# Kernel tuning notes

Hardware: AMD Instinct MI355X
Metric: run time of the kernel (lower is better)

The kernel has to match this reference:

```python
import jax, jax.numpy as jnp
import numpy as np

MULTI_N_NUM = 2  # hardcoded in FCR.__init__
EPS = 1e-07


def setup_inputs() -> dict:
    key = jax.random.key(0)
    ka, kp, kn, ki = jax.random.split(key, 4)
    B, C, H, W = 32, 3, 256, 256
    a = jax.random.normal(ka, (B, C, H, W), dtype=jnp.float32)
    p = jax.random.normal(kp, (B, C, H, W), dtype=jnp.float32)
    n = jax.random.normal(kn, (B, C, H, W), dtype=jnp.float32)
    # sample_with_j(B, 2, i) -> [i, random j != i]; deterministic materialization
    offs = jax.random.randint(ki, (B, MULTI_N_NUM - 1), 1, B)  # in [1, B-1]
    base = jnp.arange(B, dtype=jnp.int64)
    other = (base[:, None] + offs.astype(jnp.int64)) % B
    neg_idx = jnp.concatenate([base[:, None], other], axis=1)  # [B, 2]
    return {"a": a, "p": p, "n": n, "neg_idx": neg_idx}


def reference(a, p, n, neg_idx):
    # FFT2 over the last two dims -> complex64
    a_fft = jnp.fft.fft2(a)
    p_fft = jnp.fft.fft2(p)
    n_fft = jnp.fft.fft2(n)
    # d_ap[i] = mean |a_fft[i] - p_fft[i]| over (C, H, W)
    d_ap = jnp.mean(jnp.abs(a_fft - p_fft), axis=(1, 2, 3))  # [B]
    # d_an[i, k] = mean |a_fft[i] - n_fft[neg_idx[i, k]]|
    n_gather = n_fft[neg_idx]                                  # [B, K, C, H, W]
    d_an = jnp.mean(jnp.abs(a_fft[:, None] - n_gather), axis=(2, 3, 4))  # [B, K]
    contrastive = jnp.sum(d_ap[:, None] / (d_an + EPS))
    return contrastive / (MULTI_N_NUM * a.shape[0])
```

## Files before the change

### kernel.cpp

```cpp
#include <hip/hip_runtime.h>
#include <hip/hip_fp16.h>
#include <math.h>

#define PIDX(e) ((e) + ((e) >> 4))

#define WAVE_SYNC()                          \
    do {                                     \
        __builtin_amdgcn_wave_barrier();     \
        asm volatile("" ::: "memory");       \
    } while (0)

__device__ __forceinline__ float2 cadd(float2 a, float2 b) { return {a.x + b.x, a.y + b.y}; }
__device__ __forceinline__ float2 csub(float2 a, float2 b) { return {a.x - b.x, a.y - b.y}; }
__device__ __forceinline__ float2 cmul(float2 a, float2 b) {
    return {a.x * b.x - a.y * b.y, a.x * b.y + a.y * b.x};
}
__device__ __forceinline__ float2 shfl64(float2 v, int src) {
    return {__shfl(v.x, src), __shfl(v.y, src)};
}

#define BFLY4(c0, c1, c2, c3, d0, d1, d2, d3)            \
    {                                                    \
        float2 sa = cadd(c0, c2);                        \
        float2 sb = csub(c0, c2);                        \
        float2 sc = cadd(c1, c3);                        \
        float2 sd = {(c1).y - (c3).y, (c3).x - (c1).x}; \
        d0 = cadd(sa, sc);                               \
        d1 = cadd(sb, sd);                               \
        d2 = csub(sa, sc);                               \
        d3 = csub(sb, sd);                               \
    }

struct Tw {
    float2 w1, w2, w3;
};
__device__ __forceinline__ Tw make_tw(int idx) {
    const float ang = -0.024543692606170259f * (float)idx;
    float sy, cx;
    __sincosf(ang, &sy, &cx);
    Tw tw;
    tw.w1 = {cx, sy};
    tw.w2 = cmul(tw.w1, tw.w1);
    tw.w3 = cmul(tw.w2, tw.w1);
    return tw;
}

__device__ __forceinline__ void fft_stage0(float2 z0, float2 z1, float2 z2, float2 z3, float2* X,
                                           int t, const Tw& tw) {
    float2 d0, d1, d2, d3;
    BFLY4(z0, z1, z2, z3, d0, d1, d2, d3);
    const int ob = t << 2;
    X[PIDX(ob)] = d0;
    X[PIDX(ob + 1)] = cmul(tw.w1, d1);
    X[PIDX(ob + 2)] = cmul(tw.w2, d2);
    X[PIDX(ob + 3)] = cmul(tw.w3, d3);
    WAVE_SYNC();
}

template <int SH>
__device__ __forceinline__ void fft_stage_mid(float2* X, int t, const Tw& tw) {
    float2 c0 = X[PIDX(t)];
    float2 c1 = X[PIDX(t + 64)];
    float2 c2 = X[PIDX(t + 128)];
    float2 c3 = X[PIDX(t + 192)];
    WAVE_SYNC();
    float2 d0, d1, d2, d3;
    BFLY4(c0, c1, c2, c3, d0, d1, d2, d3);
    const int mm = 1 << SH;
    const int jj = t >> SH;
    const int kk = t & (mm - 1);
    const int ob = kk + 4 * mm * jj;
    X[PIDX(ob)] = d0;
    X[PIDX(ob + mm)] = cmul(tw.w1, d1);
    X[PIDX(ob + 2 * mm)] = cmul(tw.w2, d2);
    X[PIDX(ob + 3 * mm)] = cmul(tw.w3, d3);
    WAVE_SYNC();
}

__device__ __forceinline__ void fft_stage3_reg(float2* X, int t, float2& d0, float2& d1,
                                               float2& d2, float2& d3) {
    float2 c0 = X[PIDX(t)];
    float2 c1 = X[PIDX(t + 64)];
    float2 c2 = X[PIDX(t + 128)];
    float2 c3 = X[PIDX(t + 192)];
    WAVE_SYNC();
    BFLY4(c0, c1, c2, c3, d0, d1, d2, d3);
}

__device__ __forceinline__ void load16(const float* __restrict__ abase,
                                       const float* __restrict__ sbase, int r, int t, float* a0,
                                       float* a1, float* s0, float* s1) {
#pragma unroll
    for (int q = 0; q < 4; ++q) {
        a0[q] = abase[(r << 8) + t + (q << 6)];
        a1[q] = abase[((r + 1) << 8) + t + (q << 6)];
        s0[q] = sbase[(r << 8) + t + (q << 6)];
        s1[q] = sbase[((r + 1) << 8) + t + (q << 6)];
    }
}

__global__ __launch_bounds__(256) void k_rowfft(const float* __restrict__ A,
                                                const float* __restrict__ P,
                                                const float* __restrict__ N,
                                                const int* __restrict__ negIdx,
                                                __half2* __restrict__ ws, int img0) {
    __shared__ float2 Xb[4][272];
    __shared__ __half2 outT[128 * 33];

    const int img = img0 + blockIdx.y;
    const int pair = img / 3;
    const int ch = img - pair * 3;
    int i, jn;
    const float* S;
    if (pair < 32) {
        i = pair;
        jn = pair;
        S = P;
    } else {
        const int t2 = pair - 32;
        i = t2 >> 1;
        jn = negIdx[(i << 1) + (t2 & 1)];
        S = N;
    }
    const float* abase = A + ((size_t)(i * 3 + ch) << 16);
    const float* sbase = S + ((size_t)(jn * 3 + ch) << 16);

    const int tid = threadIdx.x;
    const int w = tid >> 6;
    const int t = tid & 63;
    const int r0 = blockIdx.x * 32;

    const Tw tw0 = make_tw(t);
    const Tw tw1 = make_tw(t & ~3);
    const Tw tw2 = make_tw(t & ~15);
    const int ridx = (64 - t) & 63;

    float pa0[4], pa1[4], ps0[4], ps1[4];
    load16(abase, sbase, r0 + 2 * w, t, pa0, pa1, ps0, ps1);

    for (int it = 0; it < 4; ++it) {
        const int slot = 2 * (it * 4 + w);
        float2 z[4];
#pragma unroll
        for (int q = 0; q < 4; ++q) z[q] = {pa0[q] - ps0[q], pa1[q] - ps1[q]};
        if (it < 3) load16(abase, sbase, r0 + 2 * ((it + 1) * 4 + w), t, pa0, pa1, ps0, ps1);
        fft_stage0(z[0], z[1], z[2], z[3], Xb[w], t, tw0);
        fft_stage_mid<2>(Xb[w], t, tw1);
        fft_stage_mid<4>(Xb[w], t, tw2);
        float2 d0, d1, d2, d3;
        fft_stage3_reg(Xb[w], t, d0, d1, d2, d3);
        const float2 m3 = shfl64(d3, ridx);
        const float2 m2 = shfl64(d2, ridx);
        if (t == 0) {
            outT[slot] = __floats2half2_rn(d0.x, d2.x);
            outT[slot + 1] = __floats2half2_rn(d0.y, d2.y);
        } else {
            outT[t * 33 + slot] = __floats2half2_rn(0.5f * (d0.x + m3.x), 0.5f * (d0.y - m3.y));
            outT[t * 33 + slot + 1] =
                __floats2half2_rn(0.5f * (d0.y + m3.y), -0.5f * (d0.x - m3.x));
        }
        {
            const int v = t + 64;
            const float2 mm2 = (t == 0) ? d3 : m2;
            outT[v * 33 + slot] = __floats2half2_rn(0.5f * (d1.x + mm2.x), 0.5f * (d1.y - mm2.y));
            outT[v * 33 + slot + 1] =
                __floats2half2_rn(0.5f * (d1.y + mm2.y), -0.5f * (d1.x - mm2.x));
        }
        WAVE_SYNC();
    }

    __syncthreads();

    __half2* g = ws + (size_t)blockIdx.y * (128 * 256);
    for (int e = tid; e < 128 * 8; e += 256) {
        const int v = e >> 3, rl4 = (e & 7) << 2;
        float4 val;
        __half2* vp = (__half2*)&val;
#pragma unroll
        for (int k = 0; k < 4; ++k) vp[k] = outT[v * 33 + rl4 + k];
        *(float4*)(g + v * 256 + r0 + rl4) = val;
    }
}

__global__ __launch_bounds__(256) void k_colfft(const __half2* __restrict__ ws,
                                                float* __restrict__ partial, int img0) {
    __shared__ float2 Xb[4][272];
    __shared__ float wsum[4];
    const int tid = threadIdx.x;
    const int w = tid >> 6, t = tid & 63;
    const int vbase = blockIdx.x * 16 + w * 4;
    const __half2* gimg = ws + (size_t)blockIdx.y * (128 * 256);

    const Tw tw0 = make_tw(t);
    const Tw tw1 = make_tw(t & ~3);
    const Tw tw2 = make_tw(t & ~15);

    float acc = 0.f;
    __half2 cur[4], nxt[4];
#pragma unroll
    for (int q = 0; q < 4; ++q) cur[q] = gimg[(size_t)vbase * 256 + t + (q << 6)];
    for (int j = 0; j < 4; ++j) {
        const int v = vbase + j;
        if (j < 3) {
#pragma unroll
            for (int q = 0; q < 4; ++q) nxt[q] = gimg[(size_t)(v + 1) * 256 + t + (q << 6)];
        }
        float2 z[4];
#pragma unroll
        for (int q = 0; q < 4; ++q) z[q] = __half22float2(cur[q]);
        fft_stage0(z[0], z[1], z[2], z[3], Xb[w], t, tw0);
        fft_stage_mid<2>(Xb[w], t, tw1);
        fft_stage_mid<4>(Xb[w], t, tw2);
        float2 d0, d1, d2, d3;
        fft_stage3_reg(Xb[w], t, d0, d1, d2, d3);
        float ssum = 0.f;
        if (v == 0) {
            Xb[w][PIDX(t)] = d0;
            Xb[w][PIDX(t + 64)] = d1;
            Xb[w][PIDX(t + 128)] = d2;
            Xb[w][PIDX(t + 192)] = d3;
            WAVE_SYNC();
#pragma unroll
            for (int q = 0; q < 4; ++q) {
                const int u = t + 64 * q;
                const float2 zu = Xb[w][PIDX(u)];
                const float2 zm = Xb[w][PIDX((256 - u) & 255)];
                const float ax = 0.5f * (zu.x + zm.x), ay = 0.5f * (zu.y - zm.y);
                const float bx = 0.5f * (zu.y + zm.y), by = -0.5f * (zu.x - zm.x);
                ssum += sqrtf(ax * ax + ay * ay) + sqrtf(bx * bx + by * by);
            }
        } else {
            ssum = 2.f * (sqrtf(d0.x * d0.x + d0.y * d0.y) + sqrtf(d1.x * d1.x + d1.y * d1.y) +
                          sqrtf(d2.x * d2.x + d2.y * d2.y) + sqrtf(d3.x * d3.x + d3.y * d3.y));
        }
        acc += ssum;
#pragma unroll
        for (int q = 0; q < 4; ++q) cur[q] = nxt[q];
        WAVE_SYNC();
    }
#pragma unroll
    for (int off = 32; off; off >>= 1) acc += __shfl_down(acc, off);
    if (t == 0) wsum[w] = acc;
    __syncthreads();
    if (tid == 0) {
        const int img = img0 + blockIdx.y;
        partial[img * 8 + blockIdx.x] = wsum[0] + wsum[1] + wsum[2] + wsum[3];
    }
}

__global__ void k_final(const float* __restrict__ partial, float* __restrict__ out) {
    __shared__ float ps[96];
    const int t = threadIdx.x;
    if (t < 96) {
        float s = 0.f;
        const float* p = partial + t * 24;
        for (int e = 0; e < 24; ++e) s += p[e];
        ps[t] = s;
    }
    __syncthreads();
    if (t < 64) {
        const float inv = 1.f / 196608.f;
        const float dap = ps[t >> 1] * inv;
        const float dan = ps[32 + t] * inv + 1e-7f;
        float val = dap / dan;
#pragma unroll
        for (int off = 32; off; off >>= 1) val += __shfl_down(val, off);
        if (t == 0) out[0] = val * (1.f / 64.f);
    }
}

extern "C" void kernel_launch(void* const* d_in, const int* in_sizes, int n_in,
                              void* d_out, int out_size, void* d_ws, size_t ws_size,
                              hipStream_t stream) {
    const float* A = (const float*)d_in[0];
    const float* P = (const float*)d_in[1];
    const float* N = (const float*)d_in[2];
    const int* negIdx = (const int*)d_in[3];

    float* partial = (float*)d_ws;
    __half2* inter = (__half2*)((char*)d_ws + 40960);
    const size_t perImg = (size_t)128 * 256 * sizeof(__half2);
    size_t avail = ws_size > 40960 ? ws_size - 40960 : 0;
    int cap = (int)(avail / perImg);
    if (cap > 288) cap = 288;
    if (cap < 1) cap = 1;

    for (int img0 = 0; img0 < 288; img0 += cap) {
        const int nimg = (288 - img0 < cap) ? (288 - img0) : cap;
        dim3 g1(8, nimg);
        k_rowfft<<<g1, dim3(256), 0, stream>>>(A, P, N, negIdx, inter, img0);
        dim3 g2(8, nimg);
        k_colfft<<<g2, dim3(256), 0, stream>>>(inter, partial, img0);
    }
    k_final<<<1, 128, 0, stream>>>(partial, (float*)d_out);
}
```

Baseline: 45.72 us.

## Fuse row and column FFT into one per-image kernel using LDS spectrum

Merges the row-FFT and column-FFT kernels into one kernel where each 512-thread block handles a whole image. The half-precision intermediate spectrum is kept in shared memory (about 131 KB) rather than written to and re-read from global workspace, and the partial sums shrink to one per image. This removes the global round trip and a kernel launch, but only 288 blocks run with very large LDS use, so occupancy is at most one block per CU and the column loads no longer prefetch ahead.

```diff
diff --git a/kernel.cpp b/kernel.cpp
--- a/kernel.cpp
+++ b/kernel.cpp
@@ -99,15 +99,16 @@
     }
 }
 
-__global__ __launch_bounds__(256) void k_rowfft(const float* __restrict__ A,
-                                                const float* __restrict__ P,
-                                                const float* __restrict__ N,
-                                                const int* __restrict__ negIdx,
-                                                __half2* __restrict__ ws, int img0) {
-    __shared__ float2 Xb[4][272];
-    __shared__ __half2 outT[128 * 33];
-
-    const int img = img0 + blockIdx.y;
+__global__ __launch_bounds__(512) void k_fused(const float* __restrict__ A,
+                                               const float* __restrict__ P,
+                                               const float* __restrict__ N,
+                                               const int* __restrict__ negIdx,
+                                               float* __restrict__ partial) {
+    __shared__ __half2 spec[128 * 257];
+    __shared__ float2 Xb[8][272];
+    __shared__ float wsum[8];
+
+    const int img = blockIdx.x;
     const int pair = img / 3;
     const int ch = img - pair * 3;
     int i, jn;
@@ -128,7 +129,6 @@
     const int tid = threadIdx.x;
     const int w = tid >> 6;
     const int t = tid & 63;
-    const int r0 = blockIdx.x * 32;
 
     const Tw tw0 = make_tw(t);
     const Tw tw1 = make_tw(t & ~3);
@@ -136,14 +136,14 @@
     const int ridx = (64 - t) & 63;
 
     float pa0[4], pa1[4], ps0[4], ps1[4];
-    load16(abase, sbase, r0 + 2 * w, t, pa0, pa1, ps0, ps1);
-
-    for (int it = 0; it < 4; ++it) {
-        const int slot = 2 * (it * 4 + w);
+    load16(abase, sbase, 2 * w, t, pa0, pa1, ps0, ps1);
+
+    for (int it = 0; it < 16; ++it) {
+        const int p = it * 8 + w;
         float2 z[4];
 #pragma unroll
         for (int q = 0; q < 4; ++q) z[q] = {pa0[q] - ps0[q], pa1[q] - ps1[q]};
-        if (it < 3) load16(abase, sbase, r0 + 2 * ((it + 1) * 4 + w), t, pa0, pa1, ps0, ps1);
+        if (it < 15) load16(abase, sbase, 2 * ((it + 1) * 8 + w), t, pa0, pa1, ps0, ps1);
         fft_stage0(z[0], z[1], z[2], z[3], Xb[w], t, tw0);
         fft_stage_mid<2>(Xb[w], t, tw1);
         fft_stage_mid<4>(Xb[w], t, tw2);
@@ -151,19 +151,20 @@
         fft_stage3_reg(Xb[w], t, d0, d1, d2, d3);
         const float2 m3 = shfl64(d3, ridx);
         const float2 m2 = shfl64(d2, ridx);
+        const int r = 2 * p;
         if (t == 0) {
-            outT[slot] = __floats2half2_rn(d0.x, d2.x);
-            outT[slot + 1] = __floats2half2_rn(d0.y, d2.y);
+            spec[r] = __floats2half2_rn(d0.x, d2.x);
+            spec[r + 1] = __floats2half2_rn(d0.y, d2.y);
         } else {
-            outT[t * 33 + slot] = __floats2half2_rn(0.5f * (d0.x + m3.x), 0.5f * (d0.y - m3.y));
-            outT[t * 33 + slot + 1] =
+            spec[t * 257 + r] = __floats2half2_rn(0.5f * (d0.x + m3.x), 0.5f * (d0.y - m3.y));
+            spec[t * 257 + r + 1] =
                 __floats2half2_rn(0.5f * (d0.y + m3.y), -0.5f * (d0.x - m3.x));
         }
         {
             const int v = t + 64;
             const float2 mm2 = (t == 0) ? d3 : m2;
-            outT[v * 33 + slot] = __floats2half2_rn(0.5f * (d1.x + mm2.x), 0.5f * (d1.y - mm2.y));
-            outT[v * 33 + slot + 1] =
+            spec[v * 257 + r] = __floats2half2_rn(0.5f * (d1.x + mm2.x), 0.5f * (d1.y - mm2.y));
+            spec[v * 257 + r + 1] =
                 __floats2half2_rn(0.5f * (d1.y + mm2.y), -0.5f * (d1.x - mm2.x));
         }
         WAVE_SYNC();
@@ -171,43 +172,12 @@
 
     __syncthreads();
 
-    __half2* g = ws + (size_t)blockIdx.y * (128 * 256);
-    for (int e = tid; e < 128 * 8; e += 256) {
-        const int v = e >> 3, rl4 = (e & 7) << 2;
-        float4 val;
-        __half2* vp = (__half2*)&val;
-#pragma unroll
-        for (int k = 0; k < 4; ++k) vp[k] = outT[v * 33 + rl4 + k];
-        *(float4*)(g + v * 256 + r0 + rl4) = val;
-    }
-}
-
-__global__ __launch_bounds__(256) void k_colfft(const __half2* __restrict__ ws,
-                                                float* __restrict__ partial, int img0) {
-    __shared__ float2 Xb[4][272];
-    __shared__ float wsum[4];
-    const int tid = threadIdx.x;
-    const int w = tid >> 6, t = tid & 63;
-    const int vbase = blockIdx.x * 16 + w * 4;
-    const __half2* gimg = ws + (size_t)blockIdx.y * (128 * 256);
-
-    const Tw tw0 = make_tw(t);
-    const Tw tw1 = make_tw(t & ~3);
-    const Tw tw2 = make_tw(t & ~15);
-
     float acc = 0.f;
-    __half2 cur[4], nxt[4];
-#pragma unroll
-    for (int q = 0; q < 4; ++q) cur[q] = gimg[(size_t)vbase * 256 + t + (q << 6)];
-    for (int j = 0; j < 4; ++j) {
-        const int v = vbase + j;
-        if (j < 3) {
-#pragma unroll
-            for (int q = 0; q < 4; ++q) nxt[q] = gimg[(size_t)(v + 1) * 256 + t + (q << 6)];
-        }
+    for (int it = 0; it < 16; ++it) {
+        const int v = it * 8 + w;
         float2 z[4];
 #pragma unroll
-        for (int q = 0; q < 4; ++q) z[q] = __half22float2(cur[q]);
+        for (int q = 0; q < 4; ++q) z[q] = __half22float2(spec[v * 257 + t + (q << 6)]);
         fft_stage0(z[0], z[1], z[2], z[3], Xb[w], t, tw0);
         fft_stage_mid<2>(Xb[w], t, tw1);
         fft_stage_mid<4>(Xb[w], t, tw2);
@@ -234,8 +204,6 @@
                           sqrtf(d2.x * d2.x + d2.y * d2.y) + sqrtf(d3.x * d3.x + d3.y * d3.y));
         }
         acc += ssum;
-#pragma unroll
-        for (int q = 0; q < 4; ++q) cur[q] = nxt[q];
         WAVE_SYNC();
     }
 #pragma unroll
@@ -243,20 +211,17 @@
     if (t == 0) wsum[w] = acc;
     __syncthreads();
     if (tid == 0) {
-        const int img = img0 + blockIdx.y;
-        partial[img * 8 + blockIdx.x] = wsum[0] + wsum[1] + wsum[2] + wsum[3];
+        float s = 0.f;
+#pragma unroll
+        for (int q = 0; q < 8; ++q) s += wsum[q];
+        partial[img] = s;
     }
 }
 
 __global__ void k_final(const float* __restrict__ partial, float* __restrict__ out) {
     __shared__ float ps[96];
     const int t = threadIdx.x;
-    if (t < 96) {
-        float s = 0.f;
-        const float* p = partial + t * 24;
-        for (int e = 0; e < 24; ++e) s += p[e];
-        ps[t] = s;
-    }
+    if (t < 96) ps[t] = partial[3 * t] + partial[3 * t + 1] + partial[3 * t + 2];
     __syncthreads();
     if (t < 64) {
         const float inv = 1.f / 196608.f;
@@ -278,19 +243,7 @@
     const int* negIdx = (const int*)d_in[3];
 
     float* partial = (float*)d_ws;
-    __half2* inter = (__half2*)((char*)d_ws + 40960);
-    const size_t perImg = (size_t)128 * 256 * sizeof(__half2);
-    size_t avail = ws_size > 40960 ? ws_size - 40960 : 0;
-    int cap = (int)(avail / perImg);
-    if (cap > 288) cap = 288;
-    if (cap < 1) cap = 1;
-
-    for (int img0 = 0; img0 < 288; img0 += cap) {
-        const int nimg = (288 - img0 < cap) ? (288 - img0) : cap;
-        dim3 g1(8, nimg);
-        k_rowfft<<<g1, dim3(256), 0, stream>>>(A, P, N, negIdx, inter, img0);
-        dim3 g2(8, nimg);
-        k_colfft<<<g2, dim3(256), 0, stream>>>(inter, partial, img0);
-    }
+
+    k_fused<<<dim3(288), dim3(512), 0, stream>>>(A, P, N, negIdx, partial);
     k_final<<<1, 128, 0, stream>>>(partial, (float*)d_out);
 }
```

Result: slower. 70.05 us (+53.2%).

## Fold final reduction into column FFT via last-block atomic; widen row FFT blocks

Applied to the files above, without the earlier changes.

Removes the separate k_final launch. Each column-FFT block now bumps a global counter after writing its partial, and the last block to finish performs the final reduction and writes the output. The row-FFT kernel goes from 256 to 512 threads (8 waves, 2 iterations instead of 4) and resets the counter at its start. This saves a kernel launch and raises parallelism per row block, at the cost of an atomic per column block and more shared memory per row block.

```diff
diff --git a/kernel.cpp b/kernel.cpp
--- a/kernel.cpp
+++ b/kernel.cpp
@@ -3,6 +3,9 @@
 #include <math.h>
 
 #define PIDX(e) ((e) + ((e) >> 4))
+
+#define N_IMG 288
+#define COLBLK_TOTAL (8 * N_IMG)
 
 #define WAVE_SYNC()                          \
     do {                                     \
@@ -99,13 +102,16 @@
     }
 }
 
-__global__ __launch_bounds__(256) void k_rowfft(const float* __restrict__ A,
-                                                const float* __restrict__ P,
-                                                const float* __restrict__ N,
-                                                const int* __restrict__ negIdx,
-                                                __half2* __restrict__ ws, int img0) {
-    __shared__ float2 Xb[4][272];
+__global__ __launch_bounds__(512, 8) void k_rowfft(const float* __restrict__ A,
+                                                   const float* __restrict__ P,
+                                                   const float* __restrict__ N,
+                                                   const int* __restrict__ negIdx,
+                                                   __half2* __restrict__ ws, int img0,
+                                                   int* __restrict__ counter) {
+    __shared__ float2 Xb[8][272];
     __shared__ __half2 outT[128 * 33];
+
+    if (img0 == 0 && blockIdx.x == 0 && blockIdx.y == 0 && threadIdx.x == 0) *counter = 0;
 
     const int img = img0 + blockIdx.y;
     const int pair = img / 3;
@@ -138,12 +144,12 @@
     float pa0[4], pa1[4], ps0[4], ps1[4];
     load16(abase, sbase, r0 + 2 * w, t, pa0, pa1, ps0, ps1);
 
-    for (int it = 0; it < 4; ++it) {
-        const int slot = 2 * (it * 4 + w);
+    for (int it = 0; it < 2; ++it) {
+        const int slot = 2 * (it * 8 + w);
         float2 z[4];
 #pragma unroll
         for (int q = 0; q < 4; ++q) z[q] = {pa0[q] - ps0[q], pa1[q] - ps1[q]};
-        if (it < 3) load16(abase, sbase, r0 + 2 * ((it + 1) * 4 + w), t, pa0, pa1, ps0, ps1);
+        if (it < 1) load16(abase, sbase, r0 + 2 * ((it + 1) * 8 + w), t, pa0, pa1, ps0, ps1);
         fft_stage0(z[0], z[1], z[2], z[3], Xb[w], t, tw0);
         fft_stage_mid<2>(Xb[w], t, tw1);
         fft_stage_mid<4>(Xb[w], t, tw2);
@@ -172,7 +178,7 @@
     __syncthreads();
 
     __half2* g = ws + (size_t)blockIdx.y * (128 * 256);
-    for (int e = tid; e < 128 * 8; e += 256) {
+    for (int e = tid; e < 128 * 8; e += 512) {
         const int v = e >> 3, rl4 = (e & 7) << 2;
         float4 val;
         __half2* vp = (__half2*)&val;
@@ -183,9 +189,12 @@
 }
 
 __global__ __launch_bounds__(256) void k_colfft(const __half2* __restrict__ ws,
-                                                float* __restrict__ partial, int img0) {
+                                                float* __restrict__ partial, int img0,
+                                                int* __restrict__ counter,
+                                                float* __restrict__ out) {
     __shared__ float2 Xb[4][272];
     __shared__ float wsum[4];
+    __shared__ int isLast;
     const int tid = threadIdx.x;
     const int w = tid >> 6, t = tid & 63;
     const int vbase = blockIdx.x * 16 + w * 4;
@@ -245,27 +254,31 @@
     if (tid == 0) {
         const int img = img0 + blockIdx.y;
         partial[img * 8 + blockIdx.x] = wsum[0] + wsum[1] + wsum[2] + wsum[3];
-    }
-}
-
-__global__ void k_final(const float* __restrict__ partial, float* __restrict__ out) {
-    __shared__ float ps[96];
-    const int t = threadIdx.x;
-    if (t < 96) {
-        float s = 0.f;
-        const float* p = partial + t * 24;
-        for (int e = 0; e < 24; ++e) s += p[e];
-        ps[t] = s;
+        __threadfence();
+        const int old = atomicAdd(counter, 1);
+        isLast = (old == COLBLK_TOTAL - 1) ? 1 : 0;
     }
     __syncthreads();
-    if (t < 64) {
-        const float inv = 1.f / 196608.f;
-        const float dap = ps[t >> 1] * inv;
-        const float dan = ps[32 + t] * inv + 1e-7f;
-        float val = dap / dan;
-#pragma unroll
-        for (int off = 32; off; off >>= 1) val += __shfl_down(val, off);
-        if (t == 0) out[0] = val * (1.f / 64.f);
+    if (isLast) {
+        __shared__ float ps[96];
+        if (tid == 0) __threadfence();
+        __syncthreads();
+        if (tid < 96) {
+            float s = 0.f;
+            const float* p = partial + tid * 24;
+            for (int e = 0; e < 24; ++e) s += p[e];
+            ps[tid] = s;
+        }
+        __syncthreads();
+        if (tid < 64) {
+            const float inv = 1.f / 196608.f;
+            const float dap = ps[tid >> 1] * inv;
+            const float dan = ps[32 + tid] * inv + 1e-7f;
+            float val = dap / dan;
+#pragma unroll
+            for (int off = 32; off; off >>= 1) val += __shfl_down(val, off);
+            if (tid == 0) out[0] = val * (1.f / 64.f);
+        }
     }
 }
 
@@ -278,19 +291,19 @@
     const int* negIdx = (const int*)d_in[3];
 
     float* partial = (float*)d_ws;
+    int* counter = (int*)((char*)d_ws + 9216);
     __half2* inter = (__half2*)((char*)d_ws + 40960);
     const size_t perImg = (size_t)128 * 256 * sizeof(__half2);
     size_t avail = ws_size > 40960 ? ws_size - 40960 : 0;
     int cap = (int)(avail / perImg);
-    if (cap > 288) cap = 288;
+    if (cap > N_IMG) cap = N_IMG;
     if (cap < 1) cap = 1;
 
-    for (int img0 = 0; img0 < 288; img0 += cap) {
-        const int nimg = (288 - img0 < cap) ? (288 - img0) : cap;
+    for (int img0 = 0; img0 < N_IMG; img0 += cap) {
+        const int nimg = (N_IMG - img0 < cap) ? (N_IMG - img0) : cap;
         dim3 g1(8, nimg);
-        k_rowfft<<<g1, dim3(256), 0, stream>>>(A, P, N, negIdx, inter, img0);
+        k_rowfft<<<g1, dim3(512), 0, stream>>>(A, P, N, negIdx, inter, img0, counter);
         dim3 g2(8, nimg);
-        k_colfft<<<g2, dim3(256), 0, stream>>>(inter, partial, img0);
-    }
-    k_final<<<1, 128, 0, stream>>>(partial, (float*)d_out);
-}
+        k_colfft<<<g2, dim3(256), 0, stream>>>(inter, partial, img0, counter, (float*)d_out);
+    }
+}
```

Measured after the change: 134.0 us. +193.1%, slower.

## Interleave two FFTs per wave and double row-FFT grid for more ILP

Applied to the files above, without the earlier changes.

Each wave now runs two independent 256-point FFTs in lockstep, with separate LDS buffers, so the LDS loads and butterflies of one can hide the latency of the other. The row kernel handles 16 rows per block instead of 32 and doubles its grid, adding parallelism. The column kernel issues all four column loads up front and fully unrolls into two paired passes. The cost is more registers and twice the LDS per wave, which could lower occupancy, and the row kernel writes narrower 16-row output segments.

```diff
diff --git a/kernel.cpp b/kernel.cpp
--- a/kernel.cpp
+++ b/kernel.cpp
@@ -45,46 +45,58 @@
     return tw;
 }
 
-__device__ __forceinline__ void fft_stage0(float2 z0, float2 z1, float2 z2, float2 z3, float2* X,
-                                           int t, const Tw& tw) {
-    float2 d0, d1, d2, d3;
-    BFLY4(z0, z1, z2, z3, d0, d1, d2, d3);
+
+__device__ __forceinline__ void stage0_pair(const float2* zA, const float2* zB, float2* XA,
+                                            float2* XB, int t, const Tw& tw) {
+    float2 a0, a1, a2, a3, b0, b1, b2, b3;
+    BFLY4(zA[0], zA[1], zA[2], zA[3], a0, a1, a2, a3);
+    BFLY4(zB[0], zB[1], zB[2], zB[3], b0, b1, b2, b3);
     const int ob = t << 2;
-    X[PIDX(ob)] = d0;
-    X[PIDX(ob + 1)] = cmul(tw.w1, d1);
-    X[PIDX(ob + 2)] = cmul(tw.w2, d2);
-    X[PIDX(ob + 3)] = cmul(tw.w3, d3);
+    XA[PIDX(ob)] = a0;
+    XA[PIDX(ob + 1)] = cmul(tw.w1, a1);
+    XA[PIDX(ob + 2)] = cmul(tw.w2, a2);
+    XA[PIDX(ob + 3)] = cmul(tw.w3, a3);
+    XB[PIDX(ob)] = b0;
+    XB[PIDX(ob + 1)] = cmul(tw.w1, b1);
+    XB[PIDX(ob + 2)] = cmul(tw.w2, b2);
+    XB[PIDX(ob + 3)] = cmul(tw.w3, b3);
     WAVE_SYNC();
 }
 
 template <int SH>
-__device__ __forceinline__ void fft_stage_mid(float2* X, int t, const Tw& tw) {
-    float2 c0 = X[PIDX(t)];
-    float2 c1 = X[PIDX(t + 64)];
-    float2 c2 = X[PIDX(t + 128)];
-    float2 c3 = X[PIDX(t + 192)];
+__device__ __forceinline__ void stage_mid_pair(float2* XA, float2* XB, int t, const Tw& tw) {
+    float2 cA0 = XA[PIDX(t)], cA1 = XA[PIDX(t + 64)];
+    float2 cA2 = XA[PIDX(t + 128)], cA3 = XA[PIDX(t + 192)];
+    float2 cB0 = XB[PIDX(t)], cB1 = XB[PIDX(t + 64)];
+    float2 cB2 = XB[PIDX(t + 128)], cB3 = XB[PIDX(t + 192)];
     WAVE_SYNC();
-    float2 d0, d1, d2, d3;
-    BFLY4(c0, c1, c2, c3, d0, d1, d2, d3);
+    float2 a0, a1, a2, a3, b0, b1, b2, b3;
+    BFLY4(cA0, cA1, cA2, cA3, a0, a1, a2, a3);
+    BFLY4(cB0, cB1, cB2, cB3, b0, b1, b2, b3);
     const int mm = 1 << SH;
     const int jj = t >> SH;
     const int kk = t & (mm - 1);
     const int ob = kk + 4 * mm * jj;
-    X[PIDX(ob)] = d0;
-    X[PIDX(ob + mm)] = cmul(tw.w1, d1);
-    X[PIDX(ob + 2 * mm)] = cmul(tw.w2, d2);
-    X[PIDX(ob + 3 * mm)] = cmul(tw.w3, d3);
+    XA[PIDX(ob)] = a0;
+    XA[PIDX(ob + mm)] = cmul(tw.w1, a1);
+    XA[PIDX(ob + 2 * mm)] = cmul(tw.w2, a2);
+    XA[PIDX(ob + 3 * mm)] = cmul(tw.w3, a3);
+    XB[PIDX(ob)] = b0;
+    XB[PIDX(ob + mm)] = cmul(tw.w1, b1);
+    XB[PIDX(ob + 2 * mm)] = cmul(tw.w2, b2);
+    XB[PIDX(ob + 3 * mm)] = cmul(tw.w3, b3);
     WAVE_SYNC();
 }
 
-__device__ __forceinline__ void fft_stage3_reg(float2* X, int t, float2& d0, float2& d1,
-                                               float2& d2, float2& d3) {
-    float2 c0 = X[PIDX(t)];
-    float2 c1 = X[PIDX(t + 64)];
-    float2 c2 = X[PIDX(t + 128)];
-    float2 c3 = X[PIDX(t + 192)];
+__device__ __forceinline__ void stage3_pair(float2* XA, float2* XB, int t, float2* dA,
+                                            float2* dB) {
+    float2 cA0 = XA[PIDX(t)], cA1 = XA[PIDX(t + 64)];
+    float2 cA2 = XA[PIDX(t + 128)], cA3 = XA[PIDX(t + 192)];
+    float2 cB0 = XB[PIDX(t)], cB1 = XB[PIDX(t + 64)];
+    float2 cB2 = XB[PIDX(t + 128)], cB3 = XB[PIDX(t + 192)];
     WAVE_SYNC();
-    BFLY4(c0, c1, c2, c3, d0, d1, d2, d3);
+    BFLY4(cA0, cA1, cA2, cA3, dA[0], dA[1], dA[2], dA[3]);
+    BFLY4(cB0, cB1, cB2, cB3, dB[0], dB[1], dB[2], dB[3]);
 }
 
 __device__ __forceinline__ void load16(const float* __restrict__ abase,
@@ -104,8 +116,8 @@
                                                 const float* __restrict__ N,
                                                 const int* __restrict__ negIdx,
                                                 __half2* __restrict__ ws, int img0) {
-    __shared__ float2 Xb[4][272];
-    __shared__ __half2 outT[128 * 33];
+    __shared__ float2 Xb[4][2][272];
+    __shared__ __half2 outT[128 * 17];
 
     const int img = img0 + blockIdx.y;
     const int pair = img / 3;
@@ -128,63 +140,73 @@
     const int tid = threadIdx.x;
     const int w = tid >> 6;
     const int t = tid & 63;
-    const int r0 = blockIdx.x * 32;
+    const int r0 = blockIdx.x * 16;
 
     const Tw tw0 = make_tw(t);
     const Tw tw1 = make_tw(t & ~3);
     const Tw tw2 = make_tw(t & ~15);
     const int ridx = (64 - t) & 63;
 
-    float pa0[4], pa1[4], ps0[4], ps1[4];
-    load16(abase, sbase, r0 + 2 * w, t, pa0, pa1, ps0, ps1);
-
-    for (int it = 0; it < 4; ++it) {
-        const int slot = 2 * (it * 4 + w);
-        float2 z[4];
-#pragma unroll
-        for (int q = 0; q < 4; ++q) z[q] = {pa0[q] - ps0[q], pa1[q] - ps1[q]};
-        if (it < 3) load16(abase, sbase, r0 + 2 * ((it + 1) * 4 + w), t, pa0, pa1, ps0, ps1);
-        fft_stage0(z[0], z[1], z[2], z[3], Xb[w], t, tw0);
-        fft_stage_mid<2>(Xb[w], t, tw1);
-        fft_stage_mid<4>(Xb[w], t, tw2);
-        float2 d0, d1, d2, d3;
-        fft_stage3_reg(Xb[w], t, d0, d1, d2, d3);
-        const float2 m3 = shfl64(d3, ridx);
-        const float2 m2 = shfl64(d2, ridx);
+    float a0A[4], a1A[4], s0A[4], s1A[4];
+    float a0B[4], a1B[4], s0B[4], s1B[4];
+    load16(abase, sbase, r0 + 4 * w, t, a0A, a1A, s0A, s1A);
+    load16(abase, sbase, r0 + 4 * w + 2, t, a0B, a1B, s0B, s1B);
+
+    float2 zA[4], zB[4];
+#pragma unroll
+    for (int q = 0; q < 4; ++q) {
+        zA[q] = {a0A[q] - s0A[q], a1A[q] - s1A[q]};
+        zB[q] = {a0B[q] - s0B[q], a1B[q] - s1B[q]};
+    }
+    float2* XA = Xb[w][0];
+    float2* XB = Xb[w][1];
+    stage0_pair(zA, zB, XA, XB, t, tw0);
+    stage_mid_pair<2>(XA, XB, t, tw1);
+    stage_mid_pair<4>(XA, XB, t, tw2);
+    float2 dA[4], dB[4];
+    stage3_pair(XA, XB, t, dA, dB);
+
+#pragma unroll
+    for (int f = 0; f < 2; ++f) {
+        const float2* d = f ? dB : dA;
+        const int slot = 4 * w + 2 * f;
+        const float2 m3 = shfl64(d[3], ridx);
+        const float2 m2 = shfl64(d[2], ridx);
         if (t == 0) {
-            outT[slot] = __floats2half2_rn(d0.x, d2.x);
-            outT[slot + 1] = __floats2half2_rn(d0.y, d2.y);
+            outT[slot] = __floats2half2_rn(d[0].x, d[2].x);
+            outT[slot + 1] = __floats2half2_rn(d[0].y, d[2].y);
         } else {
-            outT[t * 33 + slot] = __floats2half2_rn(0.5f * (d0.x + m3.x), 0.5f * (d0.y - m3.y));
-            outT[t * 33 + slot + 1] =
-                __floats2half2_rn(0.5f * (d0.y + m3.y), -0.5f * (d0.x - m3.x));
+            outT[t * 17 + slot] =
+                __floats2half2_rn(0.5f * (d[0].x + m3.x), 0.5f * (d[0].y - m3.y));
+            outT[t * 17 + slot + 1] =
+                __floats2half2_rn(0.5f * (d[0].y + m3.y), -0.5f * (d[0].x - m3.x));
         }
         {
             const int v = t + 64;
-            const float2 mm2 = (t == 0) ? d3 : m2;
-            outT[v * 33 + slot] = __floats2half2_rn(0.5f * (d1.x + mm2.x), 0.5f * (d1.y - mm2.y));
-            outT[v * 33 + slot + 1] =
-                __floats2half2_rn(0.5f * (d1.y + mm2.y), -0.5f * (d1.x - mm2.x));
+            const float2 mm2 = (t == 0) ? d[3] : m2;
+            outT[v * 17 + slot] =
+                __floats2half2_rn(0.5f * (d[1].x + mm2.x), 0.5f * (d[1].y - mm2.y));
+            outT[v * 17 + slot + 1] =
+                __floats2half2_rn(0.5f * (d[1].y + mm2.y), -0.5f * (d[1].x - mm2.x));
         }
-        WAVE_SYNC();
     }
 
     __syncthreads();
 
     __half2* g = ws + (size_t)blockIdx.y * (128 * 256);
-    for (int e = tid; e < 128 * 8; e += 256) {
-        const int v = e >> 3, rl4 = (e & 7) << 2;
+    for (int e = tid; e < 128 * 4; e += 256) {
+        const int v = e >> 2, rl4 = (e & 3) << 2;
         float4 val;
         __half2* vp = (__half2*)&val;
 #pragma unroll
-        for (int k = 0; k < 4; ++k) vp[k] = outT[v * 33 + rl4 + k];
+        for (int k = 0; k < 4; ++k) vp[k] = outT[v * 17 + rl4 + k];
         *(float4*)(g + v * 256 + r0 + rl4) = val;
     }
 }
 
 __global__ __launch_bounds__(256) void k_colfft(const __half2* __restrict__ ws,
                                                 float* __restrict__ partial, int img0) {
-    __shared__ float2 Xb[4][272];
+    __shared__ float2 Xb[4][2][272];
     __shared__ float wsum[4];
     const int tid = threadIdx.x;
     const int w = tid >> 6, t = tid & 63;
@@ -195,49 +217,77 @@
     const Tw tw1 = make_tw(t & ~3);
     const Tw tw2 = make_tw(t & ~15);
 
+    float2* XA = Xb[w][0];
+    float2* XB = Xb[w][1];
+
+    __half2 cA[4], cB[4], nA[4], nB[4];
+#pragma unroll
+    for (int q = 0; q < 4; ++q) {
+        cA[q] = gimg[(size_t)vbase * 256 + t + (q << 6)];
+        cB[q] = gimg[(size_t)(vbase + 1) * 256 + t + (q << 6)];
+        nA[q] = gimg[(size_t)(vbase + 2) * 256 + t + (q << 6)];
+        nB[q] = gimg[(size_t)(vbase + 3) * 256 + t + (q << 6)];
+    }
+
     float acc = 0.f;
-    __half2 cur[4], nxt[4];
-#pragma unroll
-    for (int q = 0; q < 4; ++q) cur[q] = gimg[(size_t)vbase * 256 + t + (q << 6)];
-    for (int j = 0; j < 4; ++j) {
-        const int v = vbase + j;
-        if (j < 3) {
-#pragma unroll
-            for (int q = 0; q < 4; ++q) nxt[q] = gimg[(size_t)(v + 1) * 256 + t + (q << 6)];
-        }
-        float2 z[4];
-#pragma unroll
-        for (int q = 0; q < 4; ++q) z[q] = __half22float2(cur[q]);
-        fft_stage0(z[0], z[1], z[2], z[3], Xb[w], t, tw0);
-        fft_stage_mid<2>(Xb[w], t, tw1);
-        fft_stage_mid<4>(Xb[w], t, tw2);
-        float2 d0, d1, d2, d3;
-        fft_stage3_reg(Xb[w], t, d0, d1, d2, d3);
+    float2 zA[4], zB[4], dA[4], dB[4];
+
+#pragma unroll
+    for (int q = 0; q < 4; ++q) {
+        zA[q] = __half22float2(cA[q]);
+        zB[q] = __half22float2(cB[q]);
+    }
+    stage0_pair(zA, zB, XA, XB, t, tw0);
+    stage_mid_pair<2>(XA, XB, t, tw1);
+    stage_mid_pair<4>(XA, XB, t, tw2);
+    stage3_pair(XA, XB, t, dA, dB);
+    if (vbase == 0) {
+        XA[PIDX(t)] = dA[0];
+        XA[PIDX(t + 64)] = dA[1];
+        XA[PIDX(t + 128)] = dA[2];
+        XA[PIDX(t + 192)] = dA[3];
+        WAVE_SYNC();
         float ssum = 0.f;
-        if (v == 0) {
-            Xb[w][PIDX(t)] = d0;
-            Xb[w][PIDX(t + 64)] = d1;
-            Xb[w][PIDX(t + 128)] = d2;
-            Xb[w][PIDX(t + 192)] = d3;
-            WAVE_SYNC();
-#pragma unroll
-            for (int q = 0; q < 4; ++q) {
-                const int u = t + 64 * q;
-                const float2 zu = Xb[w][PIDX(u)];
-                const float2 zm = Xb[w][PIDX((256 - u) & 255)];
-                const float ax = 0.5f * (zu.x + zm.x), ay = 0.5f * (zu.y - zm.y);
-                const float bx = 0.5f * (zu.y + zm.y), by = -0.5f * (zu.x - zm.x);
-                ssum += sqrtf(ax * ax + ay * ay) + sqrtf(bx * bx + by * by);
-            }
-        } else {
-            ssum = 2.f * (sqrtf(d0.x * d0.x + d0.y * d0.y) + sqrtf(d1.x * d1.x + d1.y * d1.y) +
-                          sqrtf(d2.x * d2.x + d2.y * d2.y) + sqrtf(d3.x * d3.x + d3.y * d3.y));
+#pragma unroll
+        for (int q = 0; q < 4; ++q) {
+            const int u = t + 64 * q;
+            const float2 zu = XA[PIDX(u)];
+            const float2 zm = XA[PIDX((256 - u) & 255)];
+            const float ax = 0.5f * (zu.x + zm.x), ay = 0.5f * (zu.y - zm.y);
+            const float bx = 0.5f * (zu.y + zm.y), by = -0.5f * (zu.x - zm.x);
+            ssum += sqrtf(ax * ax + ay * ay) + sqrtf(bx * bx + by * by);
         }
         acc += ssum;
-#pragma unroll
-        for (int q = 0; q < 4; ++q) cur[q] = nxt[q];
         WAVE_SYNC();
-    }
+    } else {
+        acc += 2.f * (sqrtf(dA[0].x * dA[0].x + dA[0].y * dA[0].y) +
+                      sqrtf(dA[1].x * dA[1].x + dA[1].y * dA[1].y) +
+                      sqrtf(dA[2].x * dA[2].x + dA[2].y * dA[2].y) +
+                      sqrtf(dA[3].x * dA[3].x + dA[3].y * dA[3].y));
+    }
+    acc += 2.f * (sqrtf(dB[0].x * dB[0].x + dB[0].y * dB[0].y) +
+                  sqrtf(dB[1].x * dB[1].x + dB[1].y * dB[1].y) +
+                  sqrtf(dB[2].x * dB[2].x + dB[2].y * dB[2].y) +
+                  sqrtf(dB[3].x * dB[3].x + dB[3].y * dB[3].y));
+
+#pragma unroll
+    for (int q = 0; q < 4; ++q) {
+        zA[q] = __half22float2(nA[q]);
+        zB[q] = __half22float2(nB[q]);
+    }
+    stage0_pair(zA, zB, XA, XB, t, tw0);
+    stage_mid_pair<2>(XA, XB, t, tw1);
+    stage_mid_pair<4>(XA, XB, t, tw2);
+    stage3_pair(XA, XB, t, dA, dB);
+    acc += 2.f * (sqrtf(dA[0].x * dA[0].x + dA[0].y * dA[0].y) +
+                  sqrtf(dA[1].x * dA[1].x + dA[1].y * dA[1].y) +
+                  sqrtf(dA[2].x * dA[2].x + dA[2].y * dA[2].y) +
+                  sqrtf(dA[3].x * dA[3].x + dA[3].y * dA[3].y));
+    acc += 2.f * (sqrtf(dB[0].x * dB[0].x + dB[0].y * dB[0].y) +
+                  sqrtf(dB[1].x * dB[1].x + dB[1].y * dB[1].y) +
+                  sqrtf(dB[2].x * dB[2].x + dB[2].y * dB[2].y) +
+                  sqrtf(dB[3].x * dB[3].x + dB[3].y * dB[3].y));
+
 #pragma unroll
     for (int off = 32; off; off >>= 1) acc += __shfl_down(acc, off);
     if (t == 0) wsum[w] = acc;
@@ -287,7 +337,7 @@
 
     for (int img0 = 0; img0 < 288; img0 += cap) {
         const int nimg = (288 - img0 < cap) ? (288 - img0) : cap;
-        dim3 g1(8, nimg);
+        dim3 g1(16, nimg);
         k_rowfft<<<g1, dim3(256), 0, stream>>>(A, P, N, negIdx, inter, img0);
         dim3 g2(8, nimg);
         k_colfft<<<g2, dim3(256), 0, stream>>>(inter, partial, img0);
```

After: 48.06 us. 5.1% more time.
